# Kernel optimization log

Hardware: AMD Instinct MI355X
Metric: run time of the kernel (lower is better)

The kernel has to match this reference:

```python
import jax, jax.numpy as jnp
import numpy as np

N_NODES = 100000
N_EDGES = 1600000
D = 64
BN_EPS = 1e-5


def setup_inputs() -> dict:
    key = jax.random.key(0)
    ks = jax.random.split(key, 10)
    s = 1.0 / np.sqrt(D)
    return {
        "features": jax.random.normal(ks[0], (N_NODES, D), dtype=jnp.float32),
        "src": jax.random.randint(ks[1], (N_EDGES,), 0, N_NODES, dtype=jnp.int32),
        "dst": jax.random.randint(ks[2], (N_EDGES,), 0, N_NODES, dtype=jnp.int32),
        "eps": jnp.zeros((), dtype=jnp.float32),
        "W1": jax.random.uniform(ks[3], (D, D), jnp.float32, -s, s),
        "b1": jax.random.uniform(ks[4], (D,), jnp.float32, -s, s),
        "W2": jax.random.uniform(ks[5], (D, D), jnp.float32, -s, s),
        "b2": jax.random.uniform(ks[6], (D,), jnp.float32, -s, s),
        "gamma": jnp.ones((D,), dtype=jnp.float32),
        "beta": jnp.zeros((D,), dtype=jnp.float32),
    }


def reference(features, src, dst, eps, W1, b1, W2, b2, gamma, beta):
    h_in = features
    # message passing: gather src node features, scatter-sum to dst (fn.copy_u + fn.sum)
    neigh = jax.ops.segment_sum(features[src], dst, num_segments=N_NODES)  # [N, D]
    # eps-weighted self term
    h = (1.0 + eps) * features + neigh
    # apply_func MLP: Linear -> ReLU -> Linear
    h = jnp.maximum(h @ W1 + b1, 0.0) @ W2 + b2
    # BatchNorm1d over nodes (training-mode batch statistics)
    mean = jnp.mean(h, axis=0)
    var = jnp.var(h, axis=0)
    h = (h - mean) * jax.lax.rsqrt(var + BN_EPS) * gamma + beta
    # activation
    h = jnp.maximum(h, 0.0)
    # residual (indim == outdim)
    h = h_in + h
    # dropout p=0 -> identity
    return h
```

## Files before the change

kernel.cpp:

```cpp
#include <hip/hip_runtime.h>
#include <hip/hip_fp16.h>

#define N_NODES 100000
#define N_EDGES 1600000
#define D 64
#define BN_EPS 1e-5f
#define NBKT 256
#define NPB 391
#define BKT_CAP 8192
#define SORT_T 1024

__global__ __launch_bounds__(256) void bucket_k(
    const int* __restrict__ src, const int* __restrict__ dst,
    int* __restrict__ bkt_cnt, int2* __restrict__ bktbuf)
{
    __shared__ int h[NBKT], base[NBKT], cur[NBKT];
    const int t = threadIdx.x;
    if (t < NBKT) { h[t] = 0; cur[t] = 0; }
    __syncthreads();
    const int e0 = blockIdx.x * 4096;
    int s[16], d[16], b[16];
    #pragma unroll
    for (int i = 0; i < 16; ++i) {
        int e = e0 + i * 256 + t;
        if (e < N_EDGES) {
            s[i] = src[e];
            d[i] = dst[e];
            b[i] = d[i] / NPB;
            atomicAdd(&h[b[i]], 1);
        } else {
            b[i] = -1;
        }
    }
    __syncthreads();
    if (t < NBKT) base[t] = atomicAdd(&bkt_cnt[t], h[t]);
    __syncthreads();
    #pragma unroll
    for (int i = 0; i < 16; ++i) {
        if (b[i] >= 0) {
            int p = atomicAdd(&cur[b[i]], 1);
            bktbuf[(size_t)b[i] * BKT_CAP + base[b[i]] + p] = make_int2(s[i], d[i]);
        }
    }
}

__global__ __launch_bounds__(SORT_T) void sort_k(
    const int2* __restrict__ bktbuf, const int* __restrict__ bkt_cnt,
    int* __restrict__ rowptr, int* __restrict__ col)
{
    __shared__ int h[NPB];
    __shared__ int cur[NPB];
    __shared__ int part[SORT_T];
    __shared__ int bsc[NBKT];

    const int b = blockIdx.x;
    const int t = threadIdx.x;
    const int nb0 = b * NPB;
    const int nodes_in = min(NPB, N_NODES - nb0);
    const int cnt = bkt_cnt[b];
    const int2* buf = bktbuf + (size_t)b * BKT_CAP;

    if (t < NBKT) bsc[t] = bkt_cnt[t];
    __syncthreads();
    for (int off = 1; off < NBKT; off <<= 1) {
        int x = 0;
        if (t < NBKT) {
            x = bsc[t];
            if (t >= off) x += bsc[t - off];
        }
        __syncthreads();
        if (t < NBKT) bsc[t] = x;
        __syncthreads();
    }
    const int gbase = bsc[b] - cnt;

    if (t < NPB) h[t] = 0;
    __syncthreads();

    for (int i = t; i < cnt; i += SORT_T)
        atomicAdd(&h[buf[i].y - nb0], 1);
    __syncthreads();

    int a = (t < NPB) ? h[t] : 0;
    part[t] = a;
    __syncthreads();
    for (int off = 1; off < SORT_T; off <<= 1) {
        int x = part[t];
        int u = (t >= off) ? part[t - off] : 0;
        __syncthreads();
        part[t] = x + u;
        __syncthreads();
    }
    int excl = part[t] - a;
    if (t < NPB) {
        cur[t] = excl;
        if (t < nodes_in) rowptr[nb0 + t] = gbase + excl;
    }
    if (b == NBKT - 1 && t == 0) rowptr[N_NODES] = N_EDGES;
    __syncthreads();

    for (int i = t; i < cnt; i += SORT_T) {
        int2 r = buf[i];
        int slot = atomicAdd(&cur[r.y - nb0], 1);
        col[gbase + slot] = r.x;
    }
}

__global__ __launch_bounds__(256) void conv_k(
    const float* __restrict__ feat, __half* __restrict__ feat16)
{
    size_t i = ((size_t)blockIdx.x * 256 + threadIdx.x) * 8;
    if (i < (size_t)N_NODES * D) {
        float4 v0 = *(const float4*)(feat + i);
        float4 v1 = *(const float4*)(feat + i + 4);
        __half2 o[4];
        o[0] = __floats2half2_rn(v0.x, v0.y);
        o[1] = __floats2half2_rn(v0.z, v0.w);
        o[2] = __floats2half2_rn(v1.x, v1.y);
        o[3] = __floats2half2_rn(v1.z, v1.w);
        *(float4*)(feat16 + i) = *(float4*)o;
    }
}

__global__ __launch_bounds__(256) void gather16_k(
    const __half* __restrict__ feat16, const int* __restrict__ rowptr,
    const int* __restrict__ col, const float* __restrict__ epsp,
    __half* __restrict__ x16)
{
    int node = blockIdx.x * 4 + (threadIdx.x >> 6);
    int lane = threadIdx.x & 63;
    if (node >= N_NODES) return;
    int g = lane >> 3;
    int c = (lane & 7) << 3;
    int lo = rowptr[node];
    int hi = rowptr[node + 1];
    float a[8] = {0.f, 0.f, 0.f, 0.f, 0.f, 0.f, 0.f, 0.f};
    int e = lo + g;
    for (; e + 8 < hi; e += 16) {
        int s0 = col[e];
        int s1 = col[e + 8];
        float4 r0 = *(const float4*)(feat16 + (size_t)s0 * D + c);
        float4 r1 = *(const float4*)(feat16 + (size_t)s1 * D + c);
        const __half2* h0 = (const __half2*)&r0;
        const __half2* h1 = (const __half2*)&r1;
        #pragma unroll
        for (int i = 0; i < 4; ++i) {
            float2 f0 = __half22float2(h0[i]);
            float2 f1 = __half22float2(h1[i]);
            a[2 * i]     += f0.x + f1.x;
            a[2 * i + 1] += f0.y + f1.y;
        }
    }
    if (e < hi) {
        float4 r0 = *(const float4*)(feat16 + (size_t)col[e] * D + c);
        const __half2* h0 = (const __half2*)&r0;
        #pragma unroll
        for (int i = 0; i < 4; ++i) {
            float2 f0 = __half22float2(h0[i]);
            a[2 * i]     += f0.x;
            a[2 * i + 1] += f0.y;
        }
    }
    #pragma unroll
    for (int off = 8; off <= 32; off <<= 1)
        #pragma unroll
        for (int i = 0; i < 8; ++i)
            a[i] += __shfl_xor(a[i], off, 64);
    if (g == 0) {
        float4 rs = *(const float4*)(feat16 + (size_t)node * D + c);
        const __half2* hs = (const __half2*)&rs;
        const float epsv = 1.0f + epsp[0];
        __half2 o[4];
        #pragma unroll
        for (int i = 0; i < 4; ++i) {
            float2 fs = __half22float2(hs[i]);
            o[i] = __floats2half2_rn(fmaf(epsv, fs.x, a[2 * i]),
                                     fmaf(epsv, fs.y, a[2 * i + 1]));
        }
        *(float4*)(x16 + (size_t)node * D + c) = *(float4*)o;
    }
}

__global__ __launch_bounds__(256) void gather32_k(
    const float* __restrict__ feat, const int* __restrict__ rowptr,
    const int* __restrict__ col, const float* __restrict__ epsp,
    float* __restrict__ x)
{
    int node = blockIdx.x * 4 + (threadIdx.x >> 6);
    int lane = threadIdx.x & 63;
    if (node >= N_NODES) return;
    int g = lane >> 4;
    int c = (lane & 15) << 2;
    int lo = rowptr[node];
    int hi = rowptr[node + 1];
    float ax = 0.f, ay = 0.f, az = 0.f, aw = 0.f;
    int e = lo + g;
    for (; e + 4 < hi; e += 8) {
        int s0 = col[e];
        int s1 = col[e + 4];
        float4 v0 = *(const float4*)(feat + (size_t)s0 * D + c);
        float4 v1 = *(const float4*)(feat + (size_t)s1 * D + c);
        ax += v0.x; ay += v0.y; az += v0.z; aw += v0.w;
        ax += v1.x; ay += v1.y; az += v1.z; aw += v1.w;
    }
    if (e < hi) {
        float4 v = *(const float4*)(feat + (size_t)col[e] * D + c);
        ax += v.x; ay += v.y; az += v.z; aw += v.w;
    }
    #pragma unroll
    for (int off = 16; off <= 32; off <<= 1) {
        ax += __shfl_xor(ax, off, 64);
        ay += __shfl_xor(ay, off, 64);
        az += __shfl_xor(az, off, 64);
        aw += __shfl_xor(aw, off, 64);
    }
    if (g == 0) {
        float4 f = *(const float4*)(feat + (size_t)node * D + c);
        const float epsv = 1.0f + epsp[0];
        float4 r;
        r.x = fmaf(epsv, f.x, ax);
        r.y = fmaf(epsv, f.y, ay);
        r.z = fmaf(epsv, f.z, az);
        r.w = fmaf(epsv, f.w, aw);
        *(float4*)(x + (size_t)node * D + c) = r;
    }
}

__device__ inline void ld8(const float* p, float* o) {
    float4 a = *(const float4*)p;
    float4 b = *(const float4*)(p + 4);
    o[0] = a.x; o[1] = a.y; o[2] = a.z; o[3] = a.w;
    o[4] = b.x; o[5] = b.y; o[6] = b.z; o[7] = b.w;
}
__device__ inline void ld8(const __half* p, float* o) {
    float4 raw = *(const float4*)p;
    const __half2* h = (const __half2*)&raw;
    #pragma unroll
    for (int i = 0; i < 4; ++i) {
        float2 f = __half22float2(h[i]);
        o[2 * i] = f.x; o[2 * i + 1] = f.y;
    }
}

template <typename XT>
__global__ __launch_bounds__(256) void mlp_k(
    const XT* __restrict__ x,
    const float* __restrict__ W1, const float* __restrict__ b1,
    const float* __restrict__ W2, const float* __restrict__ b2,
    float* __restrict__ h2out, float* __restrict__ stats8)
{
    __shared__ float W1s[64 * 68];
    __shared__ float W2s[64 * 68];
    __shared__ float xs[64 * 65];
    __shared__ float b1s[64], b2s[64];

    const int t  = threadIdx.x;
    const int nb = blockIdx.x * 64;

    #pragma unroll
    for (int i = 0; i < 4; ++i) {
        int l  = t + i * 256;
        int k  = l >> 4;
        int j4 = (l & 15) << 2;
        float4 w1 = *(const float4*)(W1 + k * 64 + j4);
        float4 w2 = *(const float4*)(W2 + k * 64 + j4);
        *(float4*)(&W1s[k * 68 + j4]) = w1;
        *(float4*)(&W2s[k * 68 + j4]) = w2;
    }
    if (t < 64)       b1s[t]      = b1[t];
    else if (t < 128) b2s[t - 64] = b2[t - 64];

    #pragma unroll
    for (int i = 0; i < 2; ++i) {
        int n  = (t >> 3) + i * 32;
        int k8 = (t & 7) << 3;
        int gn = nb + n;
        float v[8] = {0.f, 0.f, 0.f, 0.f, 0.f, 0.f, 0.f, 0.f};
        if (gn < N_NODES) ld8(x + (size_t)gn * D + k8, v);
        #pragma unroll
        for (int j = 0; j < 8; ++j) xs[n * 65 + k8 + j] = v[j];
    }
    __syncthreads();

    const int n0 = (t & 15) << 2;
    const int j0 = (t >> 4) << 2;

    const float* xr0 = &xs[(n0 + 0) * 65];
    const float* xr1 = &xs[(n0 + 1) * 65];
    const float* xr2 = &xs[(n0 + 2) * 65];
    const float* xr3 = &xs[(n0 + 3) * 65];

    float acc[4][4];
    #pragma unroll
    for (int a = 0; a < 4; ++a)
        #pragma unroll
        for (int b = 0; b < 4; ++b)
            acc[a][b] = b1s[j0 + b];

    #pragma unroll 8
    for (int k = 0; k < 64; ++k) {
        const float4 w = *(const float4*)(&W1s[k * 68 + j0]);
        const float x0 = xr0[k], x1 = xr1[k], x2 = xr2[k], x3 = xr3[k];
        acc[0][0] = fmaf(x0, w.x, acc[0][0]);
        acc[0][1] = fmaf(x0, w.y, acc[0][1]);
        acc[0][2] = fmaf(x0, w.z, acc[0][2]);
        acc[0][3] = fmaf(x0, w.w, acc[0][3]);
        acc[1][0] = fmaf(x1, w.x, acc[1][0]);
        acc[1][1] = fmaf(x1, w.y, acc[1][1]);
        acc[1][2] = fmaf(x1, w.z, acc[1][2]);
        acc[1][3] = fmaf(x1, w.w, acc[1][3]);
        acc[2][0] = fmaf(x2, w.x, acc[2][0]);
        acc[2][1] = fmaf(x2, w.y, acc[2][1]);
        acc[2][2] = fmaf(x2, w.z, acc[2][2]);
        acc[2][3] = fmaf(x2, w.w, acc[2][3]);
        acc[3][0] = fmaf(x3, w.x, acc[3][0]);
        acc[3][1] = fmaf(x3, w.y, acc[3][1]);
        acc[3][2] = fmaf(x3, w.z, acc[3][2]);
        acc[3][3] = fmaf(x3, w.w, acc[3][3]);
    }

    __syncthreads();
    #pragma unroll
    for (int a = 0; a < 4; ++a)
        #pragma unroll
        for (int b = 0; b < 4; ++b)
            xs[(n0 + a) * 65 + j0 + b] = fmaxf(acc[a][b], 0.0f);
    __syncthreads();

    float acc2[4][4];
    #pragma unroll
    for (int a = 0; a < 4; ++a)
        #pragma unroll
        for (int b = 0; b < 4; ++b)
            acc2[a][b] = b2s[j0 + b];

    #pragma unroll 8
    for (int k = 0; k < 64; ++k) {
        const float4 w = *(const float4*)(&W2s[k * 68 + j0]);
        const float x0 = xr0[k], x1 = xr1[k], x2 = xr2[k], x3 = xr3[k];
        acc2[0][0] = fmaf(x0, w.x, acc2[0][0]);
        acc2[0][1] = fmaf(x0, w.y, acc2[0][1]);
        acc2[0][2] = fmaf(x0, w.z, acc2[0][2]);
        acc2[0][3] = fmaf(x0, w.w, acc2[0][3]);
        acc2[1][0] = fmaf(x1, w.x, acc2[1][0]);
        acc2[1][1] = fmaf(x1, w.y, acc2[1][1]);
        acc2[1][2] = fmaf(x1, w.z, acc2[1][2]);
        acc2[1][3] = fmaf(x1, w.w, acc2[1][3]);
        acc2[2][0] = fmaf(x2, w.x, acc2[2][0]);
        acc2[2][1] = fmaf(x2, w.y, acc2[2][1]);
        acc2[2][2] = fmaf(x2, w.z, acc2[2][2]);
        acc2[2][3] = fmaf(x2, w.w, acc2[2][3]);
        acc2[3][0] = fmaf(x3, w.x, acc2[3][0]);
        acc2[3][1] = fmaf(x3, w.y, acc2[3][1]);
        acc2[3][2] = fmaf(x3, w.z, acc2[3][2]);
        acc2[3][3] = fmaf(x3, w.w, acc2[3][3]);
    }

    float psum[4] = {0.f, 0.f, 0.f, 0.f};
    float psq[4]  = {0.f, 0.f, 0.f, 0.f};
    #pragma unroll
    for (int a = 0; a < 4; ++a) {
        int gn = nb + n0 + a;
        if (gn < N_NODES) {
            float4 hh;
            hh.x = acc2[a][0]; hh.y = acc2[a][1]; hh.z = acc2[a][2]; hh.w = acc2[a][3];
            *(float4*)(h2out + (size_t)gn * 64 + j0) = hh;
            psum[0] += hh.x; psq[0] += hh.x * hh.x;
            psum[1] += hh.y; psq[1] += hh.y * hh.y;
            psum[2] += hh.z; psq[2] += hh.z * hh.z;
            psum[3] += hh.w; psq[3] += hh.w * hh.w;
        }
    }
    #pragma unroll
    for (int off = 8; off >= 1; off >>= 1) {
        #pragma unroll
        for (int b = 0; b < 4; ++b) {
            psum[b] += __shfl_down(psum[b], off, 16);
            psq[b]  += __shfl_down(psq[b],  off, 16);
        }
    }
    if ((t & 15) == 0) {
        float* sp = stats8 + (size_t)(blockIdx.x & 7) * 128;
        #pragma unroll
        for (int b = 0; b < 4; ++b) {
            unsafeAtomicAdd(sp + j0 + b,      psum[b]);
            unsafeAtomicAdd(sp + 64 + j0 + b, psq[b]);
        }
    }
}

__global__ void bnstats_k(const float* __restrict__ stats8,
                          const float* __restrict__ gamma,
                          const float* __restrict__ beta,
                          float* __restrict__ sf)
{
    int j = threadIdx.x;
    float s = 0.f, q = 0.f;
    #pragma unroll
    for (int c = 0; c < 8; ++c) {
        s += stats8[c * 128 + j];
        q += stats8[c * 128 + 64 + j];
    }
    const float invN = 1.0f / (float)N_NODES;
    float mean  = s * invN;
    float var   = q * invN - mean * mean;
    float scale = gamma[j] * rsqrtf(var + BN_EPS);
    sf[j]      = scale;
    sf[64 + j] = beta[j] - mean * scale;
}

__global__ __launch_bounds__(256) void finish_k(
    const float* __restrict__ feat, const float* __restrict__ sf,
    float* __restrict__ out)
{
    __shared__ float scs[64], shs[64];
    if (threadIdx.x < 64) {
        scs[threadIdx.x] = sf[threadIdx.x];
        shs[threadIdx.x] = sf[64 + threadIdx.x];
    }
    __syncthreads();
    size_t i = (size_t)blockIdx.x * 256 + threadIdx.x;
    if (i < (size_t)N_NODES * D / 4) {
        int j = (int)((i * 4) & 63);
        float4 h = *(float4*)(out + i * 4);
        float4 f = *(const float4*)(feat + i * 4);
        h.x = fmaxf(fmaf(h.x, scs[j + 0], shs[j + 0]), 0.f) + f.x;
        h.y = fmaxf(fmaf(h.y, scs[j + 1], shs[j + 1]), 0.f) + f.y;
        h.z = fmaxf(fmaf(h.z, scs[j + 2], shs[j + 2]), 0.f) + f.z;
        h.w = fmaxf(fmaf(h.w, scs[j + 3], shs[j + 3]), 0.f) + f.w;
        *(float4*)(out + i * 4) = h;
    }
}

extern "C" void kernel_launch(void* const* d_in, const int* in_sizes, int n_in,
                              void* d_out, int out_size, void* d_ws, size_t ws_size,
                              hipStream_t stream)
{
    const float* feat  = (const float*)d_in[0];
    const int*   src   = (const int*)d_in[1];
    const int*   dst   = (const int*)d_in[2];
    const float* eps   = (const float*)d_in[3];
    const float* W1    = (const float*)d_in[4];
    const float* b1    = (const float*)d_in[5];
    const float* W2    = (const float*)d_in[6];
    const float* b2    = (const float*)d_in[7];
    const float* gamma = (const float*)d_in[8];
    const float* beta  = (const float*)d_in[9];
    float* out = (float*)d_out;

    const size_t BKTSZ = (size_t)NBKT * BKT_CAP * sizeof(int2);
    const size_t F16SZ = (size_t)N_NODES * D * sizeof(__half);
    const size_t X32SZ = (size_t)N_NODES * D * sizeof(float);
    const size_t COLSZ = (size_t)N_EDGES * sizeof(int);
    const size_t RPSZ  = (size_t)(N_NODES + 1) * sizeof(int);
    const size_t TAIL  = 1024 * 4 + NBKT * 4 + 128 * 4;
    const size_t need16 = BKTSZ + F16SZ + COLSZ + RPSZ + TAIL;

    if (ws_size >= need16) {
        char* p = (char*)d_ws;
        __half* x16    = (__half*)p;
        int2*   bktbuf = (int2*)p;
        __half* feat16 = (__half*)(p + BKTSZ);
        int*    col    = (int*)(p + BKTSZ + F16SZ);
        int*    rowptr = col + N_EDGES;
        float*  stats8 = (float*)(rowptr + N_NODES + 1);
        int*    bkt_cnt = (int*)(stats8 + 1024);
        float*  sf     = (float*)(bkt_cnt + NBKT);

        hipMemsetAsync(stats8, 0, 1024 * 4 + NBKT * 4, stream);
        conv_k<<<3125, 256, 0, stream>>>(feat, feat16);
        bucket_k<<<(N_EDGES + 4095) / 4096, 256, 0, stream>>>(src, dst, bkt_cnt, bktbuf);
        sort_k<<<NBKT, SORT_T, 0, stream>>>(bktbuf, bkt_cnt, rowptr, col);
        gather16_k<<<(N_NODES + 3) / 4, 256, 0, stream>>>(feat16, rowptr, col, eps, x16);
        mlp_k<__half><<<(N_NODES + 63) / 64, 256, 0, stream>>>(x16, W1, b1, W2, b2, out, stats8);
        bnstats_k<<<1, 64, 0, stream>>>(stats8, gamma, beta, sf);
        finish_k<<<(N_NODES * D / 4 + 255) / 256, 256, 0, stream>>>(feat, sf, out);
    } else {
        char* p = (char*)d_ws;
        float* x32    = (float*)p;
        int2*  bktbuf = (int2*)p;
        int*   col    = (int*)(p + X32SZ);
        int*   rowptr = col + N_EDGES;
        float* stats8 = (float*)(rowptr + N_NODES + 1);
        int*   bkt_cnt = (int*)(stats8 + 1024);
        float* sf     = (float*)(bkt_cnt + NBKT);

        hipMemsetAsync(stats8, 0, 1024 * 4 + NBKT * 4, stream);
        bucket_k<<<(N_EDGES + 4095) / 4096, 256, 0, stream>>>(src, dst, bkt_cnt, bktbuf);
        sort_k<<<NBKT, SORT_T, 0, stream>>>(bktbuf, bkt_cnt, rowptr, col);
        gather32_k<<<(N_NODES + 3) / 4, 256, 0, stream>>>(feat, rowptr, col, eps, x32);
        mlp_k<float><<<(N_NODES + 63) / 64, 256, 0, stream>>>(x32, W1, b1, W2, b2, out, stats8);
        bnstats_k<<<1, 64, 0, stream>>>(stats8, gamma, beta, sf);
        finish_k<<<(N_NODES * D / 4 + 255) / 256, 256, 0, stream>>>(feat, sf, out);
    }
}
```

Measured before the change: 236.6 us.

## Use fp16 MFMA for the MLP and store its output in fp16

```diff
diff --git a/kernel.cpp b/kernel.cpp
--- a/kernel.cpp
+++ b/kernel.cpp
@@ -9,6 +9,9 @@
 #define NPB 391
 #define BKT_CAP 8192
 #define SORT_T 1024
+
+typedef _Float16 half8 __attribute__((ext_vector_type(8)));
+typedef float f32x4 __attribute__((ext_vector_type(4)));
 
 __global__ __launch_bounds__(256) void bucket_k(
     const int* __restrict__ src, const int* __restrict__ dst,
@@ -226,25 +229,141 @@
     }
 }
 
-__device__ inline void ld8(const float* p, float* o) {
-    float4 a = *(const float4*)p;
-    float4 b = *(const float4*)(p + 4);
-    o[0] = a.x; o[1] = a.y; o[2] = a.z; o[3] = a.w;
-    o[4] = b.x; o[5] = b.y; o[6] = b.z; o[7] = b.w;
-}
-__device__ inline void ld8(const __half* p, float* o) {
-    float4 raw = *(const float4*)p;
-    const __half2* h = (const __half2*)&raw;
-    #pragma unroll
-    for (int i = 0; i < 4; ++i) {
-        float2 f = __half22float2(h[i]);
-        o[2 * i] = f.x; o[2 * i + 1] = f.y;
-    }
-}
-
-template <typename XT>
-__global__ __launch_bounds__(256) void mlp_k(
-    const XT* __restrict__ x,
+__global__ __launch_bounds__(256) void mfma_mlp_k(
+    const __half* __restrict__ x16,
+    const float* __restrict__ W1, const float* __restrict__ b1,
+    const float* __restrict__ W2, const float* __restrict__ b2,
+    __half* __restrict__ h216, float* __restrict__ stats8)
+{
+    __shared__ __align__(16) _Float16 W1T[64 * 72];
+    __shared__ __align__(16) _Float16 W2T[64 * 72];
+    __shared__ __align__(16) _Float16 xts[64 * 72];
+    __shared__ float b1s[64], b2s[64];
+
+    const int t  = threadIdx.x;
+    const int nb = blockIdx.x * 64;
+
+    {
+        const int k  = t >> 2;
+        const int n0 = (t & 3) * 16;
+        #pragma unroll
+        for (int j = 0; j < 16; j += 4) {
+            float4 w1 = *(const float4*)(W1 + k * 64 + n0 + j);
+            float4 w2 = *(const float4*)(W2 + k * 64 + n0 + j);
+            W1T[(n0 + j + 0) * 72 + k] = (_Float16)w1.x;
+            W1T[(n0 + j + 1) * 72 + k] = (_Float16)w1.y;
+            W1T[(n0 + j + 2) * 72 + k] = (_Float16)w1.z;
+            W1T[(n0 + j + 3) * 72 + k] = (_Float16)w1.w;
+            W2T[(n0 + j + 0) * 72 + k] = (_Float16)w2.x;
+            W2T[(n0 + j + 1) * 72 + k] = (_Float16)w2.y;
+            W2T[(n0 + j + 2) * 72 + k] = (_Float16)w2.z;
+            W2T[(n0 + j + 3) * 72 + k] = (_Float16)w2.w;
+        }
+    }
+    if (t < 64)       b1s[t]      = b1[t];
+    else if (t < 128) b2s[t - 64] = b2[t - 64];
+
+    {
+        const int n = t >> 2;
+        const int c = (t & 3) * 16;
+        const int gn = nb + n;
+        float4 r0 = make_float4(0.f, 0.f, 0.f, 0.f), r1 = r0;
+        if (gn < N_NODES) {
+            r0 = *(const float4*)(x16 + (size_t)gn * 64 + c);
+            r1 = *(const float4*)(x16 + (size_t)gn * 64 + c + 8);
+        }
+        *(float4*)&xts[n * 72 + c]     = r0;
+        *(float4*)&xts[n * 72 + c + 8] = r1;
+    }
+    __syncthreads();
+
+    const int w     = t >> 6;
+    const int lane  = t & 63;
+    const int m     = lane & 15;
+    const int h     = lane >> 4;
+    const int rbase = w * 16;
+
+    const _Float16* xw = &xts[(rbase + m) * 72 + h * 8];
+    half8 a0 = *(const half8*)(xw);
+    half8 a1 = *(const half8*)(xw + 32);
+
+    f32x4 acc[4];
+    #pragma unroll
+    for (int jt = 0; jt < 4; ++jt) {
+        const float bias = b1s[jt * 16 + m];
+        acc[jt] = (f32x4){bias, bias, bias, bias};
+        const _Float16* bw = &W1T[(jt * 16 + m) * 72 + h * 8];
+        half8 bf0 = *(const half8*)(bw);
+        half8 bf1 = *(const half8*)(bw + 32);
+        acc[jt] = __builtin_amdgcn_mfma_f32_16x16x32_f16(a0, bf0, acc[jt], 0, 0, 0);
+        acc[jt] = __builtin_amdgcn_mfma_f32_16x16x32_f16(a1, bf1, acc[jt], 0, 0, 0);
+    }
+
+    #pragma unroll
+    for (int jt = 0; jt < 4; ++jt)
+        #pragma unroll
+        for (int r = 0; r < 4; ++r)
+            xts[(rbase + h * 4 + r) * 72 + jt * 16 + m] =
+                (_Float16)fmaxf(acc[jt][r], 0.0f);
+    __syncthreads();
+
+    half8 c0 = *(const half8*)(xw);
+    half8 c1 = *(const half8*)(xw + 32);
+
+    f32x4 acc2[4];
+    #pragma unroll
+    for (int jt = 0; jt < 4; ++jt) {
+        const float bias = b2s[jt * 16 + m];
+        acc2[jt] = (f32x4){bias, bias, bias, bias};
+        const _Float16* bw = &W2T[(jt * 16 + m) * 72 + h * 8];
+        half8 bf0 = *(const half8*)(bw);
+        half8 bf1 = *(const half8*)(bw + 32);
+        acc2[jt] = __builtin_amdgcn_mfma_f32_16x16x32_f16(c0, bf0, acc2[jt], 0, 0, 0);
+        acc2[jt] = __builtin_amdgcn_mfma_f32_16x16x32_f16(c1, bf1, acc2[jt], 0, 0, 0);
+    }
+
+    float psums[4], psqs[4];
+    #pragma unroll
+    for (int jt = 0; jt < 4; ++jt) {
+        float ps = 0.f, pq = 0.f;
+        #pragma unroll
+        for (int r = 0; r < 4; ++r) {
+            const int row = rbase + h * 4 + r;
+            const float v = acc2[jt][r];
+            const float vv = (nb + row < N_NODES) ? v : 0.f;
+            ps += vv;
+            pq += vv * vv;
+            xts[row * 72 + jt * 16 + m] = (_Float16)v;
+        }
+        ps += __shfl_xor(ps, 16, 64); ps += __shfl_xor(ps, 32, 64);
+        pq += __shfl_xor(pq, 16, 64); pq += __shfl_xor(pq, 32, 64);
+        psums[jt] = ps; psqs[jt] = pq;
+    }
+    if (lane < 16) {
+        float* sp = stats8 + (size_t)(blockIdx.x & 7) * 128;
+        #pragma unroll
+        for (int jt = 0; jt < 4; ++jt) {
+            unsafeAtomicAdd(sp + jt * 16 + lane,      psums[jt]);
+            unsafeAtomicAdd(sp + 64 + jt * 16 + lane, psqs[jt]);
+        }
+    }
+    __syncthreads();
+
+    {
+        const int rr = lane >> 2;
+        const int cc = (lane & 3) * 16;
+        const int gn = nb + rbase + rr;
+        if (gn < N_NODES) {
+            float4 r0 = *(const float4*)&xts[(rbase + rr) * 72 + cc];
+            float4 r1 = *(const float4*)&xts[(rbase + rr) * 72 + cc + 8];
+            *(float4*)(h216 + (size_t)gn * 64 + cc)     = r0;
+            *(float4*)(h216 + (size_t)gn * 64 + cc + 8) = r1;
+        }
+    }
+}
+
+__global__ __launch_bounds__(256) void mlp32_k(
+    const float* __restrict__ x,
     const float* __restrict__ W1, const float* __restrict__ b1,
     const float* __restrict__ W2, const float* __restrict__ b2,
     float* __restrict__ h2out, float* __restrict__ stats8)
@@ -262,10 +381,8 @@
         int l  = t + i * 256;
         int k  = l >> 4;
         int j4 = (l & 15) << 2;
-        float4 w1 = *(const float4*)(W1 + k * 64 + j4);
-        float4 w2 = *(const float4*)(W2 + k * 64 + j4);
-        *(float4*)(&W1s[k * 68 + j4]) = w1;
-        *(float4*)(&W2s[k * 68 + j4]) = w2;
+        *(float4*)(&W1s[k * 68 + j4]) = *(const float4*)(W1 + k * 64 + j4);
+        *(float4*)(&W2s[k * 68 + j4]) = *(const float4*)(W2 + k * 64 + j4);
     }
     if (t < 64)       b1s[t]      = b1[t];
     else if (t < 128) b2s[t - 64] = b2[t - 64];
@@ -275,16 +392,18 @@
         int n  = (t >> 3) + i * 32;
         int k8 = (t & 7) << 3;
         int gn = nb + n;
-        float v[8] = {0.f, 0.f, 0.f, 0.f, 0.f, 0.f, 0.f, 0.f};
-        if (gn < N_NODES) ld8(x + (size_t)gn * D + k8, v);
-        #pragma unroll
-        for (int j = 0; j < 8; ++j) xs[n * 65 + k8 + j] = v[j];
+        float4 a = make_float4(0.f, 0.f, 0.f, 0.f), b = a;
+        if (gn < N_NODES) {
+            a = *(const float4*)(x + (size_t)gn * D + k8);
+            b = *(const float4*)(x + (size_t)gn * D + k8 + 4);
+        }
+        *(float4*)&xs[n * 65 + k8]     = a;
+        *(float4*)&xs[n * 65 + k8 + 4] = b;
     }
     __syncthreads();
 
     const int n0 = (t & 15) << 2;
     const int j0 = (t >> 4) << 2;
-
     const float* xr0 = &xs[(n0 + 0) * 65];
     const float* xr1 = &xs[(n0 + 1) * 65];
     const float* xr2 = &xs[(n0 + 2) * 65];
@@ -301,22 +420,14 @@
     for (int k = 0; k < 64; ++k) {
         const float4 w = *(const float4*)(&W1s[k * 68 + j0]);
         const float x0 = xr0[k], x1 = xr1[k], x2 = xr2[k], x3 = xr3[k];
-        acc[0][0] = fmaf(x0, w.x, acc[0][0]);
-        acc[0][1] = fmaf(x0, w.y, acc[0][1]);
-        acc[0][2] = fmaf(x0, w.z, acc[0][2]);
-        acc[0][3] = fmaf(x0, w.w, acc[0][3]);
-        acc[1][0] = fmaf(x1, w.x, acc[1][0]);
-        acc[1][1] = fmaf(x1, w.y, acc[1][1]);
-        acc[1][2] = fmaf(x1, w.z, acc[1][2]);
-        acc[1][3] = fmaf(x1, w.w, acc[1][3]);
-        acc[2][0] = fmaf(x2, w.x, acc[2][0]);
-        acc[2][1] = fmaf(x2, w.y, acc[2][1]);
-        acc[2][2] = fmaf(x2, w.z, acc[2][2]);
-        acc[2][3] = fmaf(x2, w.w, acc[2][3]);
-        acc[3][0] = fmaf(x3, w.x, acc[3][0]);
-        acc[3][1] = fmaf(x3, w.y, acc[3][1]);
-        acc[3][2] = fmaf(x3, w.z, acc[3][2]);
-        acc[3][3] = fmaf(x3, w.w, acc[3][3]);
+        acc[0][0] = fmaf(x0, w.x, acc[0][0]); acc[0][1] = fmaf(x0, w.y, acc[0][1]);
+        acc[0][2] = fmaf(x0, w.z, acc[0][2]); acc[0][3] = fmaf(x0, w.w, acc[0][3]);
+        acc[1][0] = fmaf(x1, w.x, acc[1][0]); acc[1][1] = fmaf(x1, w.y, acc[1][1]);
+        acc[1][2] = fmaf(x1, w.z, acc[1][2]); acc[1][3] = fmaf(x1, w.w, acc[1][3]);
+        acc[2][0] = fmaf(x2, w.x, acc[2][0]); acc[2][1] = fmaf(x2, w.y, acc[2][1]);
+        acc[2][2] = fmaf(x2, w.z, acc[2][2]); acc[2][3] = fmaf(x2, w.w, acc[2][3]);
+        acc[3][0] = fmaf(x3, w.x, acc[3][0]); acc[3][1] = fmaf(x3, w.y, acc[3][1]);
+        acc[3][2] = fmaf(x3, w.z, acc[3][2]); acc[3][3] = fmaf(x3, w.w, acc[3][3]);
     }
 
     __syncthreads();
@@ -338,22 +449,14 @@
     for (int k = 0; k < 64; ++k) {
         const float4 w = *(const float4*)(&W2s[k * 68 + j0]);
         const float x0 = xr0[k], x1 = xr1[k], x2 = xr2[k], x3 = xr3[k];
-        acc2[0][0] = fmaf(x0, w.x, acc2[0][0]);
-        acc2[0][1] = fmaf(x0, w.y, acc2[0][1]);
-        acc2[0][2] = fmaf(x0, w.z, acc2[0][2]);
-        acc2[0][3] = fmaf(x0, w.w, acc2[0][3]);
-        acc2[1][0] = fmaf(x1, w.x, acc2[1][0]);
-        acc2[1][1] = fmaf(x1, w.y, acc2[1][1]);
-        acc2[1][2] = fmaf(x1, w.z, acc2[1][2]);
-        acc2[1][3] = fmaf(x1, w.w, acc2[1][3]);
-        acc2[2][0] = fmaf(x2, w.x, acc2[2][0]);
-        acc2[2][1] = fmaf(x2, w.y, acc2[2][1]);
-        acc2[2][2] = fmaf(x2, w.z, acc2[2][2]);
-        acc2[2][3] = fmaf(x2, w.w, acc2[2][3]);
-        acc2[3][0] = fmaf(x3, w.x, acc2[3][0]);
-        acc2[3][1] = fmaf(x3, w.y, acc2[3][1]);
-        acc2[3][2] = fmaf(x3, w.z, acc2[3][2]);
-        acc2[3][3] = fmaf(x3, w.w, acc2[3][3]);
+        acc2[0][0] = fmaf(x0, w.x, acc2[0][0]); acc2[0][1] = fmaf(x0, w.y, acc2[0][1]);
+        acc2[0][2] = fmaf(x0, w.z, acc2[0][2]); acc2[0][3] = fmaf(x0, w.w, acc2[0][3]);
+        acc2[1][0] = fmaf(x1, w.x, acc2[1][0]); acc2[1][1] = fmaf(x1, w.y, acc2[1][1]);
+        acc2[1][2] = fmaf(x1, w.z, acc2[1][2]); acc2[1][3] = fmaf(x1, w.w, acc2[1][3]);
+        acc2[2][0] = fmaf(x2, w.x, acc2[2][0]); acc2[2][1] = fmaf(x2, w.y, acc2[2][1]);
+        acc2[2][2] = fmaf(x2, w.z, acc2[2][2]); acc2[2][3] = fmaf(x2, w.w, acc2[2][3]);
+        acc2[3][0] = fmaf(x3, w.x, acc2[3][0]); acc2[3][1] = fmaf(x3, w.y, acc2[3][1]);
+        acc2[3][2] = fmaf(x3, w.z, acc2[3][2]); acc2[3][3] = fmaf(x3, w.w, acc2[3][3]);
     }
 
     float psum[4] = {0.f, 0.f, 0.f, 0.f};
@@ -372,13 +475,12 @@
         }
     }
     #pragma unroll
-    for (int off = 8; off >= 1; off >>= 1) {
+    for (int off = 8; off >= 1; off >>= 1)
         #pragma unroll
         for (int b = 0; b < 4; ++b) {
             psum[b] += __shfl_down(psum[b], off, 16);
             psq[b]  += __shfl_down(psq[b],  off, 16);
         }
-    }
     if ((t & 15) == 0) {
         float* sp = stats8 + (size_t)(blockIdx.x & 7) * 128;
         #pragma unroll
@@ -407,6 +509,32 @@
     float scale = gamma[j] * rsqrtf(var + BN_EPS);
     sf[j]      = scale;
     sf[64 + j] = beta[j] - mean * scale;
+}
+
+__global__ __launch_bounds__(256) void finish16_k(
+    const float* __restrict__ feat, const __half* __restrict__ h216,
+    const float* __restrict__ sf, float* __restrict__ out)
+{
+    __shared__ float scs[64], shs[64];
+    if (threadIdx.x < 64) {
+        scs[threadIdx.x] = sf[threadIdx.x];
+        shs[threadIdx.x] = sf[64 + threadIdx.x];
+    }
+    __syncthreads();
+    size_t i = (size_t)blockIdx.x * 256 + threadIdx.x;
+    if (i < (size_t)N_NODES * D / 4) {
+        int j = (int)((i * 4) & 63);
+        const __half2* hp = (const __half2*)(h216 + i * 4);
+        float2 h0 = __half22float2(hp[0]);
+        float2 h1 = __half22float2(hp[1]);
+        float4 f = *(const float4*)(feat + i * 4);
+        float4 o;
+        o.x = fmaxf(fmaf(h0.x, scs[j + 0], shs[j + 0]), 0.f) + f.x;
+        o.y = fmaxf(fmaf(h0.y, scs[j + 1], shs[j + 1]), 0.f) + f.y;
+        o.z = fmaxf(fmaf(h1.x, scs[j + 2], shs[j + 2]), 0.f) + f.z;
+        o.w = fmaxf(fmaf(h1.y, scs[j + 3], shs[j + 3]), 0.f) + f.w;
+        *(float4*)(out + i * 4) = o;
+    }
 }
 
 __global__ __launch_bounds__(256) void finish_k(
@@ -461,6 +589,7 @@
         __half* x16    = (__half*)p;
         int2*   bktbuf = (int2*)p;
         __half* feat16 = (__half*)(p + BKTSZ);
+        __half* h216   = (__half*)(p + BKTSZ);
         int*    col    = (int*)(p + BKTSZ + F16SZ);
         int*    rowptr = col + N_EDGES;
         float*  stats8 = (float*)(rowptr + N_NODES + 1);
@@ -472,9 +601,9 @@
         bucket_k<<<(N_EDGES + 4095) / 4096, 256, 0, stream>>>(src, dst, bkt_cnt, bktbuf);
         sort_k<<<NBKT, SORT_T, 0, stream>>>(bktbuf, bkt_cnt, rowptr, col);
         gather16_k<<<(N_NODES + 3) / 4, 256, 0, stream>>>(feat16, rowptr, col, eps, x16);
-        mlp_k<__half><<<(N_NODES + 63) / 64, 256, 0, stream>>>(x16, W1, b1, W2, b2, out, stats8);
+        mfma_mlp_k<<<(N_NODES + 63) / 64, 256, 0, stream>>>(x16, W1, b1, W2, b2, h216, stats8);
         bnstats_k<<<1, 64, 0, stream>>>(stats8, gamma, beta, sf);
-        finish_k<<<(N_NODES * D / 4 + 255) / 256, 256, 0, stream>>>(feat, sf, out);
+        finish16_k<<<(N_NODES * D / 4 + 255) / 256, 256, 0, stream>>>(feat, h216, sf, out);
     } else {
         char* p = (char*)d_ws;
         float* x32    = (float*)p;
@@ -489,7 +618,7 @@
         bucket_k<<<(N_EDGES + 4095) / 4096, 256, 0, stream>>>(src, dst, bkt_cnt, bktbuf);
         sort_k<<<NBKT, SORT_T, 0, stream>>>(bktbuf, bkt_cnt, rowptr, col);
         gather32_k<<<(N_NODES + 3) / 4, 256, 0, stream>>>(feat, rowptr, col, eps, x32);
-        mlp_k<float><<<(N_NODES + 63) / 64, 256, 0, stream>>>(x32, W1, b1, W2, b2, out, stats8);
+        mlp32_k<<<(N_NODES + 63) / 64, 256, 0, stream>>>(x32, W1, b1, W2, b2, out, stats8);
         bnstats_k<<<1, 64, 0, stream>>>(stats8, gamma, beta, sf);
         finish_k<<<(N_NODES * D / 4 + 255) / 256, 256, 0, stream>>>(feat, sf, out);
     }
```

After: 243.9 us. 3.1% more time.
